# Kernel optimization log

Hardware: AMD Instinct MI355X
Metric: run time of the kernel (lower is better)

Reference implementation:

```python
import jax, jax.numpy as jnp
import numpy as np
import math

B, S, H, NH = 2, 2048, 2048, 16
D = H // NH            # head dim = 128
FF = 4 * H
EPS = 1e-5


def layer_norm(x, w, b):
    mu = jnp.mean(x, axis=-1, keepdims=True)
    var = jnp.mean((x - mu) ** 2, axis=-1, keepdims=True)
    return (x - mu) * jax.lax.rsqrt(var + EPS) * w + b


def rotate_half(x):
    # split last dim into two halves (j=2 grouping), return (-x2, x1)
    x1, x2 = jnp.split(x, 2, axis=-1)
    return jnp.concatenate((-x2, x1), axis=-1)


def rope_freqs(seq_len, dim):
    inv_freq = 1.0 / (10000.0 ** (jnp.arange(0, dim, 2, dtype=jnp.float32) / dim))
    freqs = jnp.arange(seq_len, dtype=jnp.float32)[:, None] * inv_freq[None, :]
    return jnp.concatenate((freqs, freqs), axis=-1)  # [S, D]


def setup_inputs() -> dict:
    key = jax.random.key(0)
    ks = jax.random.split(key, 8)
    sc_h = 1.0 / math.sqrt(H)
    sc_ff = 1.0 / math.sqrt(FF)
    return {
        "hidden_states": jax.random.normal(ks[0], (B, S, H), jnp.float32),
        "attention_mask": jnp.zeros((1, 1, S, S), jnp.bool_),
        "ln1_w": jnp.ones((H,), jnp.float32),
        "ln1_b": jnp.zeros((H,), jnp.float32),
        "wqkv": jax.random.uniform(ks[1], (3 * H, H), jnp.float32, -sc_h, sc_h),
        "bqkv": jnp.zeros((3 * H,), jnp.float32),
        "wdense": jax.random.uniform(ks[2], (H, H), jnp.float32, -sc_h, sc_h),
        "bdense": jnp.zeros((H,), jnp.float32),
        "ln2_w": jnp.ones((H,), jnp.float32),
        "ln2_b": jnp.zeros((H,), jnp.float32),
        "w1": jax.random.uniform(ks[3], (FF, H), jnp.float32, -sc_h, sc_h),
        "b1": jnp.zeros((FF,), jnp.float32),
        "w2": jax.random.uniform(ks[4], (H, FF), jnp.float32, -sc_ff, sc_ff),
        "b2": jnp.zeros((H,), jnp.float32),
    }


def reference(hidden_states, attention_mask, ln1_w, ln1_b, wqkv, bqkv,
              wdense, bdense, ln2_w, ln2_b, w1, b1, w2, b2):
    residual = hidden_states
    x = layer_norm(hidden_states, ln1_w, ln1_b)

    qkv = jnp.einsum('bsh,oh->bso', x, wqkv) + bqkv           # [B,S,3H]
    qkv = qkv.reshape(B, S, NH, 3 * D).transpose(0, 2, 1, 3)  # [B,NH,S,3D]
    q, k, v = jnp.split(qkv, 3, axis=-1)                      # each [B,NH,S,D]

    pos = rope_freqs(S, D)                                    # [S,D]
    cos, sin = jnp.cos(pos), jnp.sin(pos)
    q = q * cos + rotate_half(q) * sin
    k = k * cos + rotate_half(k) * sin

    scale = 1.0 / math.sqrt(D)
    scores = jnp.einsum('bhqd,bhkd->bhqk', q, k) * scale      # [B,NH,S,S]
    causal = jnp.tril(jnp.ones((S, S), jnp.bool_))
    scores = jnp.where(causal, scores.astype(jnp.float32), -1e9)
    probs = jax.nn.softmax(scores, axis=-1).astype(v.dtype)

    ctx = jnp.einsum('bhqk,bhkd->bhqd', probs, v)             # [B,NH,S,D]
    ctx = ctx.transpose(0, 2, 1, 3).reshape(B, S, H)
    attn_out = jnp.einsum('bsh,oh->bso', ctx, wdense) + bdense

    hidden = residual + attn_out
    residual = hidden
    x = layer_norm(hidden, ln2_w, ln2_b)
    inter = jax.nn.gelu(jnp.einsum('bsh,fh->bsf', x, w1) + b1, approximate=False)
    out = jnp.einsum('bsf,hf->bsh', inter, w2) + b2
    hidden = residual + out
    return (hidden, attention_mask)
```

## Files before the change

kernel.cpp:

```cpp
#include <hip/hip_runtime.h>
#include <math.h>

typedef unsigned short u16;
typedef unsigned int u32;
typedef __attribute__((ext_vector_type(8))) __bf16 bf16x8;
typedef __attribute__((ext_vector_type(4))) float f32x4;
typedef __attribute__((ext_vector_type(8))) u16 u16x8;
typedef __attribute__((ext_vector_type(4))) u16 u16x4;

#define BB 2
#define SS 2048
#define HH 2048
#define NHH 16
#define DD 128
#define FFF 8192
#define MM (BB * SS)

__device__ __forceinline__ u16 f2bf(float f) {
  u32 u = __float_as_uint(f);
  u32 r = (u + 0x7FFFu + ((u >> 16) & 1u)) >> 16;
  return (u16)r;
}
__device__ __forceinline__ float b2f(u16 h) {
  return __uint_as_float(((u32)h) << 16);
}
__device__ __forceinline__ void gll16(const void* g, void* l) {
  __builtin_amdgcn_global_load_lds((const __attribute__((address_space(1))) void*)g,
                                   (__attribute__((address_space(3))) void*)l, 16, 0, 0);
}

struct CvtArgs {
  const float* src[4];
  u16* dst[4];
  int n[4];
};
__global__ __launch_bounds__(256) void cvt_all(CvtArgs a) {
  const int seg = blockIdx.y;
  const int i = (blockIdx.x * 256 + threadIdx.x) * 4;
  if (i + 3 < a.n[seg]) {
    f32x4 v = *(const f32x4*)(a.src[seg] + i);
    u16x4 o;
    o[0] = f2bf(v[0]); o[1] = f2bf(v[1]); o[2] = f2bf(v[2]); o[3] = f2bf(v[3]);
    *(u16x4*)(a.dst[seg] + i) = o;
  }
}

__global__ __launch_bounds__(256) void ln_bf16(const float* __restrict__ x,
                                               const float* __restrict__ w,
                                               const float* __restrict__ bsh,
                                               u16* __restrict__ out) {
  const int row = blockIdx.x, tid = threadIdx.x;
  const float* xr = x + (size_t)row * HH;
  f32x4 a = ((const f32x4*)xr)[tid * 2];
  f32x4 b = ((const f32x4*)xr)[tid * 2 + 1];
  float s = a[0] + a[1] + a[2] + a[3] + b[0] + b[1] + b[2] + b[3];
  float q = a[0]*a[0] + a[1]*a[1] + a[2]*a[2] + a[3]*a[3]
          + b[0]*b[0] + b[1]*b[1] + b[2]*b[2] + b[3]*b[3];
#pragma unroll
  for (int off = 32; off > 0; off >>= 1) {
    s += __shfl_down(s, off);
    q += __shfl_down(q, off);
  }
  __shared__ float red[8];
  const int wave = tid >> 6;
  if ((tid & 63) == 0) { red[wave] = s; red[4 + wave] = q; }
  __syncthreads();
  s = red[0] + red[1] + red[2] + red[3];
  q = red[4] + red[5] + red[6] + red[7];
  const float mean = s * (1.0f / HH);
  const float var = q * (1.0f / HH) - mean * mean;
  const float rstd = 1.0f / sqrtf(var + 1e-5f);
  f32x4 w0 = ((const f32x4*)w)[tid * 2];
  f32x4 w1 = ((const f32x4*)w)[tid * 2 + 1];
  f32x4 b0 = ((const f32x4*)bsh)[tid * 2];
  f32x4 b1 = ((const f32x4*)bsh)[tid * 2 + 1];
  u16x8 o;
#pragma unroll
  for (int i = 0; i < 4; ++i) o[i] = f2bf((a[i] - mean) * rstd * w0[i] + b0[i]);
#pragma unroll
  for (int i = 0; i < 4; ++i) o[4 + i] = f2bf((b[i] - mean) * rstd * w1[i] + b1[i]);
  *(u16x8*)(out + (size_t)row * HH + tid * 8) = o;
}

template <int MODE, int DB>
__global__ __launch_bounds__(256) void gemm_bt(const u16* __restrict__ A,
                                               const u16* __restrict__ Bw,
                                               const float* __restrict__ bias,
                                               const float* resid, void* Cout,
                                               int M, int N, int K) {
  __shared__ __align__(16) u16 As[DB ? 2 : 1][128 * 64];
  __shared__ __align__(16) u16 Bs[DB ? 2 : 1][128 * 64];
  const int tid = threadIdx.x;
  const int wave = tid >> 6, lane = tid & 63;
  const int l15 = lane & 15, quad = lane >> 4;
  const int bm = blockIdx.x, bn = blockIdx.y;
  const int wm = (wave >> 1) << 6, wn = (wave & 1) << 6;

  f32x4 acc[4][4] = {};

  const int srow = (wave << 5) + (lane >> 3);
  const int sg = (lane & 7) ^ (lane >> 3);
  const u16* aptr = A + (size_t)(bm * 128 + srow) * K + sg * 8;
  const u16* bptr = Bw + (size_t)(bn * 128 + srow) * K + sg * 8;

  auto stage = [&](int buf) {
#pragma unroll
    for (int i = 0; i < 4; ++i)
      gll16(aptr + (size_t)i * 8 * K, &As[buf][(wave * 4 + i) * 512]);
#pragma unroll
    for (int i = 0; i < 4; ++i)
      gll16(bptr + (size_t)i * 8 * K, &Bs[buf][(wave * 4 + i) * 512]);
    aptr += 64; bptr += 64;
  };

  auto compute = [&](int buf) {
#pragma unroll
    for (int tt = 0; tt < 2; ++tt) {
      bf16x8 af[4], bfv[4];
#pragma unroll
      for (int i = 0; i < 4; ++i) {
        const int m = wm + i * 16 + l15;
        const int n = wn + i * 16 + l15;
        const int gi = tt * 4 + quad;
        af[i] = *(const bf16x8*)&As[buf][m * 64 + ((gi ^ (m & 7)) << 3)];
        bfv[i] = *(const bf16x8*)&Bs[buf][n * 64 + ((gi ^ (n & 7)) << 3)];
      }
#pragma unroll
      for (int i = 0; i < 4; ++i)
#pragma unroll
        for (int j = 0; j < 4; ++j)
          acc[i][j] = __builtin_amdgcn_mfma_f32_16x16x32_bf16(af[i], bfv[j], acc[i][j], 0, 0, 0);
    }
  };

  const int nk = K >> 6;
  if constexpr (DB) {
    stage(0);
    for (int kt = 0; kt < nk; ++kt) {
      __syncthreads();
      if (kt + 1 < nk) stage((kt + 1) & 1);
      compute(kt & 1);
    }
  } else {
    for (int kt = 0; kt < nk; ++kt) {
      stage(0);
      __syncthreads();
      compute(0);
      __syncthreads();
    }
  }

#pragma unroll
  for (int i = 0; i < 4; ++i) {
    const int row0 = bm * 128 + wm + i * 16 + quad * 4;
#pragma unroll
    for (int j = 0; j < 4; ++j) {
      const int col = bn * 128 + wn + j * 16 + l15;
      const float bv = bias[col];
#pragma unroll
      for (int r = 0; r < 4; ++r) {
        const size_t idx = (size_t)(row0 + r) * N + col;
        float v = acc[i][j][r] + bv;
        if constexpr (MODE == 0) {
          ((u16*)Cout)[idx] = f2bf(v);
        } else if constexpr (MODE == 1) {
          ((float*)Cout)[idx] = v + resid[idx];
        } else {
          v = 0.5f * v * (1.0f + erff(v * 0.70710678118654752f));
          ((u16*)Cout)[idx] = f2bf(v);
        }
      }
    }
  }
}

__global__ __launch_bounds__(256) void rope_kernel(const u16* __restrict__ qkv,
                                                   u16* __restrict__ Qr,
                                                   u16* __restrict__ Kr) {
  const int tid = threadIdx.x;
  const int d = tid & 63;
  const int s = blockIdx.x * 4 + (tid >> 6);
  const int h = blockIdx.y, b = blockIdx.z;
  const u16* row = qkv + ((size_t)(b * SS + s)) * (3 * HH) + h * (3 * DD);
  const float q1 = b2f(row[d]),        q2 = b2f(row[d + 64]);
  const float k1 = b2f(row[DD + d]),   k2 = b2f(row[DD + d + 64]);
  const float inv = expf((float)d * -0.14391156830963714f);
  const float ang = (float)s * inv;
  const float cs = cosf(ang), sn = sinf(ang);
  const size_t o = ((size_t)(b * NHH + h) * SS + s) * DD;
  Qr[o + d]      = f2bf(q1 * cs - q2 * sn);
  Qr[o + d + 64] = f2bf(q2 * cs + q1 * sn);
  Kr[o + d]      = f2bf(k1 * cs - k2 * sn);
  Kr[o + d + 64] = f2bf(k2 * cs + k1 * sn);
}

__device__ __forceinline__ int vslot(int s, int chunk) {
  return chunk ^ (s & 7) ^ ((s >> 3) & 7);
}
__global__ __launch_bounds__(256) void vtrans(const u16* __restrict__ qkv,
                                              u16* __restrict__ Vt) {
  __shared__ __align__(16) u16 Vs[64 * 128];
  const int tid = threadIdx.x;
  const int s0 = blockIdx.x * 64;
  const int bh = blockIdx.y;
  const int b = bh >> 4, h = bh & 15;
  const u16* src = qkv + (size_t)(b * SS + s0) * (3 * HH) + h * (3 * DD) + 2 * DD;
#pragma unroll
  for (int rr = 0; rr < 4; ++rr) {
    const int task = tid + rr * 256;
    const int sr = task >> 4, c = task & 15;
    u16x8 v = *(const u16x8*)(src + (size_t)sr * (3 * HH) + c * 8);
    const int sl = (vslot(sr, c & 7) | (c & 8));
    *(u16x8*)&Vs[sr * 128 + sl * 8] = v;
  }
  __syncthreads();
#pragma unroll
  for (int rr = 0; rr < 4; ++rr) {
    const int task = tid + rr * 256;
    const int dr = task >> 3, c = task & 7;
    u16x8 o;
#pragma unroll
    for (int e = 0; e < 8; ++e) {
      const int s = c * 8 + e;
      const int sl = (vslot(s, dr >> 3 & 7) | ((dr >> 3) & 8));
      o[e] = Vs[s * 128 + sl * 8 + (dr & 7)];
    }
    *(u16x8*)(Vt + (size_t)(bh * DD + dr) * SS + s0 + c * 8) = o;
  }
}

__device__ __forceinline__ void softmax_pv(f32x4 s4[4], bool diag, int qrl0,
                                           float m_run[4], float l_run[4],
                                           f32x4 oacc[8], const u16* vtb,
                                           u16* psw, int quad, int l15) {
  const float SCL = 0.12751742904630190f;
  float pv[4][4];
  float mx[4] = {-3e38f, -3e38f, -3e38f, -3e38f};
#pragma unroll
  for (int jt = 0; jt < 4; ++jt)
#pragma unroll
    for (int r = 0; r < 4; ++r) {
      float sv = s4[jt][r] * SCL;
      if (diag && (jt * 16 + l15) > (qrl0 + r)) sv = -3e38f;
      pv[jt][r] = sv;
      mx[r] = fmaxf(mx[r], sv);
    }
#pragma unroll
  for (int r = 0; r < 4; ++r) {
    mx[r] = fmaxf(mx[r], __shfl_xor(mx[r], 1));
    mx[r] = fmaxf(mx[r], __shfl_xor(mx[r], 2));
    mx[r] = fmaxf(mx[r], __shfl_xor(mx[r], 4));
    mx[r] = fmaxf(mx[r], __shfl_xor(mx[r], 8));
  }
  float al[4];
#pragma unroll
  for (int r = 0; r < 4; ++r) {
    const float mnew = fmaxf(m_run[r], mx[r]);
    al[r] = exp2f(m_run[r] - mnew);
    m_run[r] = mnew;
  }
  float rs[4] = {0.f, 0.f, 0.f, 0.f};
#pragma unroll
  for (int jt = 0; jt < 4; ++jt)
#pragma unroll
    for (int r = 0; r < 4; ++r) {
      const float pp = exp2f(pv[jt][r] - m_run[r]);
      pv[jt][r] = pp;
      rs[r] += pp;
    }
#pragma unroll
  for (int r = 0; r < 4; ++r) {
    rs[r] += __shfl_xor(rs[r], 1);
    rs[r] += __shfl_xor(rs[r], 2);
    rs[r] += __shfl_xor(rs[r], 4);
    rs[r] += __shfl_xor(rs[r], 8);
    l_run[r] = l_run[r] * al[r] + rs[r];
  }
#pragma unroll
  for (int jn = 0; jn < 8; ++jn)
#pragma unroll
    for (int r = 0; r < 4; ++r) oacc[jn][r] *= al[r];
#pragma unroll
  for (int jt = 0; jt < 4; ++jt)
#pragma unroll
    for (int r = 0; r < 4; ++r) {
      const int qr = quad * 4 + r, key = jt * 16 + l15;
      psw[qr * 64 + (((key >> 3) ^ (qr & 7)) << 3) + (key & 7)] = f2bf(pv[jt][r]);
    }
  __threadfence_block();
#pragma unroll
  for (int t = 0; t < 2; ++t) {
    const int gg = t * 4 + quad;
    bf16x8 pf = *(const bf16x8*)&psw[l15 * 64 + ((gg ^ (l15 & 7)) << 3)];
#pragma unroll
    for (int jn = 0; jn < 8; ++jn) {
      const int nd = jn * 16 + l15;
      bf16x8 vf = *(const bf16x8*)&vtb[nd * 64 + ((gg ^ (nd & 7)) << 3)];
      oacc[jn] = __builtin_amdgcn_mfma_f32_16x16x32_bf16(pf, vf, oacc[jn], 0, 0, 0);
    }
  }
}

__global__ __launch_bounds__(256, 2) void attn_kernel(const u16* __restrict__ Q,
                                                      const u16* __restrict__ Kg,
                                                      const u16* __restrict__ Vtg,
                                                      u16* __restrict__ ctx) {
  __shared__ __align__(16) u16 Ks[2][64 * 128];
  __shared__ __align__(16) u16 Vt[2][128 * 64];
  __shared__ __align__(16) u16 Ps[4][16 * 64];
  const int tid = threadIdx.x;
  const int wave = tid >> 6, lane = tid & 63;
  const int l15 = lane & 15, quad = lane >> 4;
  const int p = blockIdx.x, h = blockIdx.y, b = blockIdx.z;
  const int qlo = p, qhi = 31 - p;
  const size_t bh = (size_t)(b * NHH + h);
  const u16* Qp = Q + bh * ((size_t)SS * DD);
  const u16* Kp = Kg + bh * ((size_t)SS * DD);
  const u16* Vp = Vtg + bh * ((size_t)DD * SS);

  bf16x8 qfl[4], qfh[4];
  {
    const u16* ql = Qp + (size_t)(qlo * 64 + wave * 16 + l15) * DD + quad * 8;
    const u16* qh = Qp + (size_t)(qhi * 64 + wave * 16 + l15) * DD + quad * 8;
#pragma unroll
    for (int t = 0; t < 4; ++t) {
      qfl[t] = *(const bf16x8*)(ql + t * 32);
      qfh[t] = *(const bf16x8*)(qh + t * 32);
    }
  }

  f32x4 oal[8] = {}, oah[8] = {};
  float ml[4] = {-3e38f, -3e38f, -3e38f, -3e38f};
  float mh[4] = {-3e38f, -3e38f, -3e38f, -3e38f};
  float ll[4] = {0.f, 0.f, 0.f, 0.f}, lh[4] = {0.f, 0.f, 0.f, 0.f};

  auto stage = [&](int kt, int bufi) {
    const int k0 = kt * 64;
#pragma unroll
    for (int i = 0; i < 4; ++i) {
      const int g = wave * 4 + i;
      const int r = g * 4 + quad;
      const int c = l15 ^ (r & 15);
      gll16(Kp + (size_t)(k0 + r) * DD + c * 8, &Ks[bufi][g * 512]);
    }
#pragma unroll
    for (int i = 0; i < 4; ++i) {
      const int g = wave * 4 + i;
      const int d = g * 8 + (lane >> 3);
      const int c = (lane & 7) ^ (d & 7);
      gll16(Vp + (size_t)d * SS + k0 + c * 8, &Vt[bufi][g * 512]);
    }
  };

  stage(0, 0);
  const int qrl0 = wave * 16 + quad * 4;
  for (int kt = 0; kt <= qhi; ++kt) {
    __syncthreads();
    const u16* ksb = Ks[kt & 1];
    const u16* vtb = Vt[kt & 1];
    if (kt < qhi) stage(kt + 1, (kt + 1) & 1);
    const bool lo = (kt <= qlo);

    f32x4 sh4[4] = {}, sl4[4] = {};
#pragma unroll
    for (int t = 0; t < 4; ++t)
#pragma unroll
      for (int jt = 0; jt < 4; ++jt) {
        const int key = jt * 16 + l15;
        bf16x8 kf = *(const bf16x8*)&ksb[key * 128 + (((t * 4 + quad) ^ (key & 15)) << 3)];
        sh4[jt] = __builtin_amdgcn_mfma_f32_16x16x32_bf16(qfh[t], kf, sh4[jt], 0, 0, 0);
        if (lo) sl4[jt] = __builtin_amdgcn_mfma_f32_16x16x32_bf16(qfl[t], kf, sl4[jt], 0, 0, 0);
      }

    softmax_pv(sh4, kt == qhi, qrl0, mh, lh, oah, vtb, Ps[wave], quad, l15);
    if (lo) softmax_pv(sl4, kt == qlo, qrl0, ml, ll, oal, vtb, Ps[wave], quad, l15);
  }

  float invh[4], invl[4];
#pragma unroll
  for (int r = 0; r < 4; ++r) { invh[r] = 1.0f / lh[r]; invl[r] = 1.0f / ll[r]; }
#pragma unroll
  for (int jn = 0; jn < 8; ++jn)
#pragma unroll
    for (int r = 0; r < 4; ++r) {
      const int col = h * DD + jn * 16 + l15;
      const int rh = qhi * 64 + qrl0 + r;
      const int rl = qlo * 64 + qrl0 + r;
      ctx[(size_t)(b * SS + rh) * HH + col] = f2bf(oah[jn][r] * invh[r]);
      ctx[(size_t)(b * SS + rl) * HH + col] = f2bf(oal[jn][r] * invl[r]);
    }
}

extern "C" void kernel_launch(void* const* d_in, const int* in_sizes, int n_in,
                              void* d_out, int out_size, void* d_ws, size_t ws_size,
                              hipStream_t stream) {
  (void)in_sizes; (void)n_in; (void)ws_size;
  const float* hidden = (const float*)d_in[0];
  const float* ln1w = (const float*)d_in[2];
  const float* ln1b = (const float*)d_in[3];
  const float* wqkv = (const float*)d_in[4];
  const float* bqkv = (const float*)d_in[5];
  const float* wdense = (const float*)d_in[6];
  const float* bdense = (const float*)d_in[7];
  const float* ln2w = (const float*)d_in[8];
  const float* ln2b = (const float*)d_in[9];
  const float* w1 = (const float*)d_in[10];
  const float* b1 = (const float*)d_in[11];
  const float* w2 = (const float*)d_in[12];
  const float* b2 = (const float*)d_in[13];

  char* ws = (char*)d_ws;
  size_t off = 0;
  auto alloc = [&](size_t elems) {
    u16* p = (u16*)(ws + off);
    off += ((elems * 2 + 255) & ~(size_t)255);
    return p;
  };
  u16* wqkvbf = alloc((size_t)3 * HH * HH);
  u16* wdbf   = alloc((size_t)HH * HH);
  u16* w1bf   = alloc((size_t)FFF * HH);
  u16* w2bf   = alloc((size_t)HH * FFF);
  u16* xbf    = alloc((size_t)MM * HH);
  u16* ctx    = alloc((size_t)MM * HH);
  u16* big    = alloc((size_t)MM * 3 * HH + 3 * (size_t)BB * NHH * SS * DD);
  u16* qkvbuf = big;
  u16* Qr = big + (size_t)MM * 3 * HH;
  u16* Kr = Qr + (size_t)BB * NHH * SS * DD;
  u16* Vtg = Kr + (size_t)BB * NHH * SS * DD;
  u16* inter = big;

  CvtArgs ca;
  ca.src[0] = wqkv;   ca.dst[0] = wqkvbf; ca.n[0] = 3 * HH * HH;
  ca.src[1] = wdense; ca.dst[1] = wdbf;   ca.n[1] = HH * HH;
  ca.src[2] = w1;     ca.dst[2] = w1bf;   ca.n[2] = FFF * HH;
  ca.src[3] = w2;     ca.dst[3] = w2bf;   ca.n[3] = HH * FFF;
  cvt_all<<<dim3((FFF * HH) / 1024, 4), 256, 0, stream>>>(ca);

  ln_bf16<<<MM, 256, 0, stream>>>(hidden, ln1w, ln1b, xbf);
  gemm_bt<0, 0><<<dim3(MM / 128, (3 * HH) / 128), 256, 0, stream>>>(
      xbf, wqkvbf, bqkv, nullptr, qkvbuf, MM, 3 * HH, HH);
  rope_kernel<<<dim3(SS / 4, NHH, BB), 256, 0, stream>>>(qkvbuf, Qr, Kr);
  vtrans<<<dim3(SS / 64, BB * NHH), 256, 0, stream>>>(qkvbuf, Vtg);
  attn_kernel<<<dim3(16, NHH, BB), 256, 0, stream>>>(Qr, Kr, Vtg, ctx);
  gemm_bt<1, 1><<<dim3(MM / 128, HH / 128), 256, 0, stream>>>(
      ctx, wdbf, bdense, hidden, d_out, MM, HH, HH);
  ln_bf16<<<MM, 256, 0, stream>>>((const float*)d_out, ln2w, ln2b, xbf);
  gemm_bt<2, 0><<<dim3(MM / 128, FFF / 128), 256, 0, stream>>>(
      xbf, w1bf, b1, nullptr, inter, MM, FFF, HH);
  gemm_bt<1, 1><<<dim3(MM / 128, HH / 128), 256, 0, stream>>>(
      inter, w2bf, b2, (const float*)d_out, d_out, MM, HH, FFF);

  const size_t hid_elems = (size_t)MM * HH;
  if ((size_t)out_size > hid_elems)
    hipMemsetAsync((char*)d_out + hid_elems * 4, 0,
                   ((size_t)out_size - hid_elems) * 4, stream);
}
```

Measured before the change: 924.8 us.

## Add 256x256 tiled 8-wave GEMM with phased prefetch for QKV and FFN1

Introduces a new GEMM kernel with 256x256 output tiles, 512 threads, double-buffered LDS, and four interleaved compute phases that each issue part of the next tile's global-to-LDS loads. It also uses XOR-swizzled LDS layout and setprio around MFMA blocks. It is used for the QKV projection and the first FFN GEMM, the two largest-N GEMMs. The aim is more data reuse per tile and better overlap of loads with MFMA work. The cost is fewer blocks (lower wave count on large-N grids) and high register and LDS pressure from 128 KB shared memory and 32 accumulators per thread.

```diff
diff --git a/kernel.cpp b/kernel.cpp
--- a/kernel.cpp
+++ b/kernel.cpp
@@ -165,6 +165,112 @@
           ((u16*)Cout)[idx] = f2bf(v);
         } else if constexpr (MODE == 1) {
           ((float*)Cout)[idx] = v + resid[idx];
+        } else {
+          v = 0.5f * v * (1.0f + erff(v * 0.70710678118654752f));
+          ((u16*)Cout)[idx] = f2bf(v);
+        }
+      }
+    }
+  }
+}
+
+#define PHASE256(QM, QN, STG, DW)                                                              \
+  do {                                                                                         \
+    bf16x8 af[4][2], bq[2][2];                                                                 \
+    _Pragma("unroll") for (int im = 0; im < 4; ++im) {                                         \
+      const int ar = wm * 128 + (QM) * 64 + im * 16 + l15;                                     \
+      _Pragma("unroll") for (int tt = 0; tt < 2; ++tt)                                         \
+          af[im][tt] = *(const bf16x8*)&as[ar * 64 + ((((tt << 2) + quad) ^ (ar & 7)) << 3)];  \
+    }                                                                                          \
+    _Pragma("unroll") for (int jn = 0; jn < 2; ++jn) {                                         \
+      const int br = wn * 64 + (QN) * 32 + jn * 16 + l15;                                      \
+      _Pragma("unroll") for (int tt = 0; tt < 2; ++tt)                                         \
+          bq[jn][tt] = *(const bf16x8*)&bs[br * 64 + ((((tt << 2) + quad) ^ (br & 7)) << 3)];  \
+    }                                                                                          \
+    STG;                                                                                       \
+    __builtin_amdgcn_s_barrier();                                                              \
+    asm volatile("s_waitcnt lgkmcnt(0)" ::: "memory");                                         \
+    __builtin_amdgcn_sched_barrier(0);                                                         \
+    __builtin_amdgcn_s_setprio(1);                                                             \
+    _Pragma("unroll") for (int tt = 0; tt < 2; ++tt)                                           \
+        _Pragma("unroll") for (int im = 0; im < 4; ++im)                                       \
+            _Pragma("unroll") for (int jn = 0; jn < 2; ++jn)                                   \
+                acc[(QM) * 4 + im][(QN) * 2 + jn] = __builtin_amdgcn_mfma_f32_16x16x32_bf16(   \
+                    af[im][tt], bq[jn][tt], acc[(QM) * 4 + im][(QN) * 2 + jn], 0, 0, 0);       \
+    __builtin_amdgcn_s_setprio(0);                                                             \
+    if (DW) {                                                                                  \
+      asm volatile("s_waitcnt vmcnt(4)" ::: "memory");                                         \
+      __builtin_amdgcn_sched_barrier(0);                                                       \
+    }                                                                                          \
+    __builtin_amdgcn_s_barrier();                                                              \
+  } while (0)
+
+template <int MODE>
+__global__ __launch_bounds__(512, 2) void gemm256(const u16* __restrict__ A,
+                                                  const u16* __restrict__ Bw,
+                                                  const float* __restrict__ bias,
+                                                  void* Cout, int M, int N, int K) {
+  __shared__ __align__(16) u16 As[2][256 * 64];
+  __shared__ __align__(16) u16 Bs[2][256 * 64];
+  const int tid = threadIdx.x;
+  const int wave = tid >> 6, lane = tid & 63;
+  const int l15 = lane & 15, quad = lane >> 4;
+  const int wm = wave >> 2, wn = wave & 3;
+  const int bm = blockIdx.x, bn = blockIdx.y;
+
+  f32x4 acc[8][4] = {};
+
+  const size_t loff = (size_t)(lane >> 3) * K + (size_t)(((lane & 7) ^ (lane >> 3)) << 3);
+  const u16* Abase = A + (size_t)(bm * 256) * K + loff;
+  const u16* Bbase = Bw + (size_t)(bn * 256) * K + loff;
+
+  auto stageA = [&](int buf, int kt, int h) {
+#pragma unroll
+    for (int i = 0; i < 2; ++i) {
+      const int c = wave * 2 + i;
+      const int rb = ((c & 8) << 4) | (h * 64 + (c & 7) * 8);
+      gll16(Abase + (size_t)rb * K + kt * 64, &As[buf][rb * 64]);
+    }
+  };
+  auto stageB = [&](int buf, int kt, int h) {
+#pragma unroll
+    for (int i = 0; i < 2; ++i) {
+      const int c = wave * 2 + i;
+      const int rb = (c >> 2) * 64 + h * 32 + (c & 3) * 8;
+      gll16(Bbase + (size_t)rb * K + kt * 64, &Bs[buf][rb * 64]);
+    }
+  };
+
+  const int nk = K >> 6;
+  stageA(0, 0, 0); stageB(0, 0, 0); stageA(0, 0, 1); stageB(0, 0, 1);
+  asm volatile("s_waitcnt vmcnt(4)" ::: "memory");
+  __builtin_amdgcn_sched_barrier(0);
+  __builtin_amdgcn_s_barrier();
+
+  for (int kt = 0; kt < nk; ++kt) {
+    const int cb = kt & 1, ob = cb ^ 1;
+    const u16* as = As[cb];
+    const u16* bs = Bs[cb];
+    const bool pf = (kt + 1 < nk);
+    PHASE256(0, 0, { if (pf) stageA(ob, kt + 1, 0); }, 1);
+    PHASE256(1, 0, { if (pf) stageB(ob, kt + 1, 0); }, 1);
+    PHASE256(1, 1, { if (pf) stageA(ob, kt + 1, 1); }, 0);
+    PHASE256(0, 1, { if (pf) stageB(ob, kt + 1, 1); }, 1);
+  }
+
+#pragma unroll
+  for (int i = 0; i < 8; ++i) {
+    const int row0 = bm * 256 + wm * 128 + (i >> 2) * 64 + (i & 3) * 16 + quad * 4;
+#pragma unroll
+    for (int j = 0; j < 4; ++j) {
+      const int col = bn * 256 + wn * 64 + (j >> 1) * 32 + (j & 1) * 16 + l15;
+      const float bv = bias[col];
+#pragma unroll
+      for (int r = 0; r < 4; ++r) {
+        const size_t idx = (size_t)(row0 + r) * N + col;
+        float v = acc[i][j][r] + bv;
+        if constexpr (MODE == 0) {
+          ((u16*)Cout)[idx] = f2bf(v);
         } else {
           v = 0.5f * v * (1.0f + erff(v * 0.70710678118654752f));
           ((u16*)Cout)[idx] = f2bf(v);
@@ -437,16 +543,16 @@
   cvt_all<<<dim3((FFF * HH) / 1024, 4), 256, 0, stream>>>(ca);
 
   ln_bf16<<<MM, 256, 0, stream>>>(hidden, ln1w, ln1b, xbf);
-  gemm_bt<0, 0><<<dim3(MM / 128, (3 * HH) / 128), 256, 0, stream>>>(
-      xbf, wqkvbf, bqkv, nullptr, qkvbuf, MM, 3 * HH, HH);
+  gemm256<0><<<dim3(MM / 256, (3 * HH) / 256), 512, 0, stream>>>(
+      xbf, wqkvbf, bqkv, qkvbuf, MM, 3 * HH, HH);
   rope_kernel<<<dim3(SS / 4, NHH, BB), 256, 0, stream>>>(qkvbuf, Qr, Kr);
   vtrans<<<dim3(SS / 64, BB * NHH), 256, 0, stream>>>(qkvbuf, Vtg);
   attn_kernel<<<dim3(16, NHH, BB), 256, 0, stream>>>(Qr, Kr, Vtg, ctx);
   gemm_bt<1, 1><<<dim3(MM / 128, HH / 128), 256, 0, stream>>>(
       ctx, wdbf, bdense, hidden, d_out, MM, HH, HH);
   ln_bf16<<<MM, 256, 0, stream>>>((const float*)d_out, ln2w, ln2b, xbf);
-  gemm_bt<2, 0><<<dim3(MM / 128, FFF / 128), 256, 0, stream>>>(
-      xbf, w1bf, b1, nullptr, inter, MM, FFF, HH);
+  gemm256<2><<<dim3(MM / 256, FFF / 256), 512, 0, stream>>>(
+      xbf, w1bf, b1, inter, MM, FFF, HH);
   gemm_bt<1, 1><<<dim3(MM / 128, HH / 128), 256, 0, stream>>>(
       inter, w2bf, b2, (const float*)d_out, d_out, MM, HH, FFF);
 
```

Measured after the change: 1.056 ms. 14.2% more time.
